# Optimization experiments

Measured on AMD Instinct MI355X. Metric: run time of the kernel, lower is better.

## Reference

```python
import jax, jax.numpy as jnp
import numpy as np

K = 499  # kernel_size


def setup_inputs() -> dict:
    key = jax.random.key(0)
    k1, k2 = jax.random.split(key)
    B, F, T = 32, 64, 8000
    # nonnegative spectrogram input, shape (B, 1, F, T)
    x = jax.random.uniform(k1, (B, 1, F, T), dtype=jnp.float32)
    a = 0.90 + 0.099 * jax.random.uniform(k2, (F,), dtype=jnp.float32)
    w = jnp.ones((F,), dtype=jnp.float32)
    return {"x": x, "a": a, "w": w}


def _build_kernel(a, w, dtype):
    # powers[f, k] = a_f ** k, k = 0..K-2
    F = a.shape[0]
    powers = a[:, None] ** jnp.arange(K - 1, dtype=dtype)  # (F, K-1)
    C = 1.0 / powers.sum(axis=1)                            # (F,)
    neg = (-C * w)[:, None] * powers                        # (F, K-1)
    # pre-flip kernel = [1, neg_0, ..., neg_{K-2}]; flipped -> [neg_{K-2}, ..., neg_0, 1]
    kern = jnp.concatenate([neg[:, ::-1], jnp.ones((F, 1), dtype)], axis=1)  # (F, K)
    return kern[:, None, :]  # (F, 1, K) OIH, groups = F


def reference(x, a, w):
    dtype = x.dtype
    kern = _build_kernel(a.astype(dtype), w.astype(dtype), dtype)
    xs = x[:, 0]  # (B, F, T)
    # replicate (edge) pad on the left by K-1 along time
    xp = jnp.pad(xs, ((0, 0), (0, 0), (K - 1, 0)), mode="edge")
    y = jax.lax.conv_general_dilated(
        xp, kern,
        window_strides=(1,), padding="VALID",
        dimension_numbers=("NCH", "OIH", "NCH"),
        feature_group_count=xs.shape[1],
    )  # (B, F, T)
    return jnp.abs(y)[:, None]  # (B, 1, F, T)
```

## Files before the change

### kernel.cpp

```cpp
#include <hip/hip_runtime.h>
#include <math.h>


constexpr int T     = 8000;
constexpr int F     = 64;
constexpr int B     = 32;
constexpr int KM1   = 498;
constexpr int CHUNK = 512;
constexpr int HALF  = 4096;
constexpr int LXN   = HALF + CHUNK;

#define DPP_F(x, ctrl, rm) \
  __builtin_bit_cast(float, __builtin_amdgcn_update_dpp(0, __builtin_bit_cast(int, (x)), (ctrl), (rm), 0xf, false))

__device__ __forceinline__ double dpow(double b, int e) {
    double r = 1.0, p = b;
    while (e) { if (e & 1) r *= p; p *= p; e >>= 1; }
    return r;
}

__device__ __forceinline__ float powi(float base, int e) {
    float r = 1.0f, p = base;
    #pragma unroll
    for (int b = 0; b < 9; ++b) { r = (e & (1 << b)) ? r * p : r; p *= p; }
    return r;
}

__device__ __forceinline__ int swz(int i) { return i ^ (((i >> 5) & 7) << 2); }

__global__ __launch_bounds__(512, 4) void willmore_scan_kernel(
    const float* __restrict__ x, const float* __restrict__ a,
    const float* __restrict__ w, float* __restrict__ out)
{
    __shared__ float lx[LXN];
    __shared__ float cb[8];

    const int tid  = threadIdx.x;
    const int cl   = tid >> 6;
    const int lane = tid & 63;
    const int row  = blockIdx.x >> 1;
    const int half = blockIdx.x & 1;
    const int f    = row & (F - 1);
    const int h0   = half * HALF;

    const float* xr   = x   + (size_t)row * T;
    float*       orow = out + (size_t)row * T;

    const int t0   = h0 + cl * CHUNK;
    const int tb_u = t0 + 8 * lane;
    const int tb   = min(tb_u, T - 8);
    const int lb   = tb - h0 + CHUNK;

    const float4 m0 = *(const float4*)(xr + tb);
    const float4 m1 = *(const float4*)(xr + tb + 4);
    float4 hv;
    if (half && tid < 128)
        hv = *(const float4*)(xr + h0 - CHUNK + 4 * tid);

    const float af    = a[f];
    const float alane = powi(af, 8 * lane);
    const float wA    = powi(af, 8 * ((lane & 15) + 1));
    const float wB    = powi(af, 8 * ((lane & 31) + 1));

    if (tid == 0) {
        const double ad     = (double)af;
        const double a498d  = dpow(ad, KM1);
        const double sumgeo = (1.0 - a498d) / (1.0 - ad);
        const double r_d    = dpow(ad, 8);
        cb[0] = (float)(-a498d);
        cb[1] = (float)(1.0 / sumgeo) * w[f];
        cb[2] = (float)r_d;
        cb[3] = (float)(r_d * r_d);
        cb[4] = (float)dpow(r_d, 4);
        cb[5] = (float)dpow(r_d, 8);
        cb[6] = (float)(1.0 / r_d);
        cb[7] = (float)sumgeo;
    }

    *(float4*)(&lx[swz(lb)])     = m0;
    *(float4*)(&lx[swz(lb + 4)]) = m1;
    if (half && tid < 128)
        *(float4*)(&lx[swz(4 * tid)]) = hv;
    __syncthreads();

    const float na498 = cb[0], g  = cb[1], r1    = cb[2], r2 = cb[3],
                r4    = cb[4], r8 = cb[5], inv_r = cb[6];

    float S;
    if (half == 0 && cl == 0) {
        S = lx[swz(CHUNK)] * cb[7];
    } else {
        const int wl = cl * CHUNK + 8 * lane;
        const float4 w0 = *(const float4*)(&lx[swz(wl)]);
        const float4 w1 = *(const float4*)(&lx[swz(wl + 4)]);
        float ws8[8] = {w0.x, w0.y, w0.z, w0.w, w1.x, w1.y, w1.z, w1.w};
        #pragma unroll
        for (int i = 0; i < 8; ++i) { if (8 * lane + i < 14) ws8[i] = 0.0f; }
        float h = ws8[0];
        #pragma unroll
        for (int i = 1; i < 8; ++i) h = fmaf(h, af, ws8[i]);
        float contrib = powi(af, 504 - 8 * lane) * h;
        #pragma unroll
        for (int s = 1; s < 64; s <<= 1) contrib += __shfl_xor(contrib, s, 64);
        S = contrib;
    }

    const int lg = tb - KM1;
    float lv[8];
    if (half == 0 && cl == 0) {
        #pragma unroll
        for (int i = 0; i < 8; ++i) lv[i] = lx[swz(max(lg + i, 0) + CHUNK)];
    } else {
        const int ll = lg - h0 + CHUNK;
        #pragma unroll
        for (int i = 0; i < 4; ++i) {
            const float2 p = *(const float2*)(&lx[swz(ll + 2 * i)]);
            lv[2 * i]     = p.x;
            lv[2 * i + 1] = p.y;
        }
    }

    const float xv[8] = {m0.x, m0.y, m0.z, m0.w, m1.x, m1.y, m1.z, m1.w};
    float u[8];
    #pragma unroll
    for (int i = 0; i < 8; ++i) u[i] = fmaf(na498, lv[i], xv[i]);

    float q = u[0];
    #pragma unroll
    for (int i = 1; i < 8; ++i) q = fmaf(q, af, u[i]);

    float G = q;
    G = fmaf(r1, DPP_F(G, 0x111, 0xf), G);
    G = fmaf(r2, DPP_F(G, 0x112, 0xf), G);
    G = fmaf(r4, DPP_F(G, 0x114, 0xf), G);
    G = fmaf(r8, DPP_F(G, 0x118, 0xf), G);
    G = fmaf(wA, DPP_F(G, 0x142, 0xa), G);
    G = fmaf(wB, DPP_F(G, 0x143, 0xc), G);

    const float E = (G - q) * inv_r;

    float s = fmaf(alane, S, E);
    float y[8];
    #pragma unroll
    for (int i = 0; i < 8; ++i) {
        y[i] = fabsf(fmaf(-g, s, xv[i]));
        s = fmaf(af, s, u[i]);
    }

    if (tb_u <= T - 8) {
        *(float4*)(orow + tb)     = make_float4(y[0], y[1], y[2], y[3]);
        *(float4*)(orow + tb + 4) = make_float4(y[4], y[5], y[6], y[7]);
    }
}

extern "C" void kernel_launch(void* const* d_in, const int* in_sizes, int n_in,
                              void* d_out, int out_size, void* d_ws, size_t ws_size,
                              hipStream_t stream) {
    const float* x = (const float*)d_in[0];
    const float* a = (const float*)d_in[1];
    const float* w = (const float*)d_in[2];
    float* out = (float*)d_out;

    hipLaunchKernelGGL(willmore_scan_kernel, dim3(B * F * 2), dim3(512), 0, stream,
                       x, a, w, out);
}
```

Baseline: 113.2 us.

## Split rows into quarter blocks with XCD-aware remap and nontemporal stores

Each row is now handled by four 256-thread blocks covering 2048 samples each, instead of two 512-thread blocks covering 4096. Block IDs are remapped so consecutive hardware blocks, which are spread across the XCDs, stay on related rows. Output stores become nontemporal. The intent is better occupancy and less LDS per block, and keeping the streaming output from polluting the cache. The cost is more redundant halo loads and more per-block setup work.

Measured after the change: 112.5 us. Within noise of the previous version (-0.6%).

```diff
diff --git a/kernel.cpp b/kernel.cpp
--- a/kernel.cpp
+++ b/kernel.cpp
@@ -7,8 +7,10 @@
 constexpr int B     = 32;
 constexpr int KM1   = 498;
 constexpr int CHUNK = 512;
-constexpr int HALF  = 4096;
-constexpr int LXN   = HALF + CHUNK;
+constexpr int QUART = 2048;
+constexpr int LXN   = QUART + CHUNK;
+
+typedef float vfloat4 __attribute__((ext_vector_type(4)));
 
 #define DPP_F(x, ctrl, rm) \
   __builtin_bit_cast(float, __builtin_amdgcn_update_dpp(0, __builtin_bit_cast(int, (x)), (ctrl), (rm), 0xf, false))
@@ -28,34 +30,37 @@
 
 __device__ __forceinline__ int swz(int i) { return i ^ (((i >> 5) & 7) << 2); }
 
-__global__ __launch_bounds__(512, 4) void willmore_scan_kernel(
+__global__ __launch_bounds__(256, 6) void willmore_scan_kernel(
     const float* __restrict__ x, const float* __restrict__ a,
     const float* __restrict__ w, float* __restrict__ out)
 {
     __shared__ float lx[LXN];
     __shared__ float cb[8];
 
+    const int bid  = blockIdx.x;
+    const int qid  = ((bid & 7) << 10) | (bid >> 3);
+
     const int tid  = threadIdx.x;
     const int cl   = tid >> 6;
     const int lane = tid & 63;
-    const int row  = blockIdx.x >> 1;
-    const int half = blockIdx.x & 1;
+    const int row  = qid >> 2;
+    const int qpos = qid & 3;
     const int f    = row & (F - 1);
-    const int h0   = half * HALF;
+    const int q0   = qpos * QUART;
 
     const float* xr   = x   + (size_t)row * T;
     float*       orow = out + (size_t)row * T;
 
-    const int t0   = h0 + cl * CHUNK;
+    const int t0   = q0 + cl * CHUNK;
     const int tb_u = t0 + 8 * lane;
     const int tb   = min(tb_u, T - 8);
-    const int lb   = tb - h0 + CHUNK;
+    const int lb   = tb - q0 + CHUNK;
 
     const float4 m0 = *(const float4*)(xr + tb);
     const float4 m1 = *(const float4*)(xr + tb + 4);
     float4 hv;
-    if (half && tid < 128)
-        hv = *(const float4*)(xr + h0 - CHUNK + 4 * tid);
+    if (qpos && tid < 128)
+        hv = *(const float4*)(xr + q0 - CHUNK + 4 * tid);
 
     const float af    = a[f];
     const float alane = powi(af, 8 * lane);
@@ -79,7 +84,7 @@
 
     *(float4*)(&lx[swz(lb)])     = m0;
     *(float4*)(&lx[swz(lb + 4)]) = m1;
-    if (half && tid < 128)
+    if (qpos && tid < 128)
         *(float4*)(&lx[swz(4 * tid)]) = hv;
     __syncthreads();
 
@@ -87,7 +92,7 @@
                 r4    = cb[4], r8 = cb[5], inv_r = cb[6];
 
     float S;
-    if (half == 0 && cl == 0) {
+    if (qpos == 0 && cl == 0) {
         S = lx[swz(CHUNK)] * cb[7];
     } else {
         const int wl = cl * CHUNK + 8 * lane;
@@ -107,11 +112,11 @@
 
     const int lg = tb - KM1;
     float lv[8];
-    if (half == 0 && cl == 0) {
+    if (qpos == 0 && cl == 0) {
         #pragma unroll
         for (int i = 0; i < 8; ++i) lv[i] = lx[swz(max(lg + i, 0) + CHUNK)];
     } else {
-        const int ll = lg - h0 + CHUNK;
+        const int ll = lg - q0 + CHUNK;
         #pragma unroll
         for (int i = 0; i < 4; ++i) {
             const float2 p = *(const float2*)(&lx[swz(ll + 2 * i)]);
@@ -148,8 +153,10 @@
     }
 
     if (tb_u <= T - 8) {
-        *(float4*)(orow + tb)     = make_float4(y[0], y[1], y[2], y[3]);
-        *(float4*)(orow + tb + 4) = make_float4(y[4], y[5], y[6], y[7]);
+        const vfloat4 o0 = {y[0], y[1], y[2], y[3]};
+        const vfloat4 o1 = {y[4], y[5], y[6], y[7]};
+        __builtin_nontemporal_store(o0, (vfloat4*)(orow + tb));
+        __builtin_nontemporal_store(o1, (vfloat4*)(orow + tb + 4));
     }
 }
 
@@ -161,6 +168,6 @@
     const float* w = (const float*)d_in[2];
     float* out = (float*)d_out;
 
-    hipLaunchKernelGGL(willmore_scan_kernel, dim3(B * F * 2), dim3(512), 0, stream,
+    hipLaunchKernelGGL(willmore_scan_kernel, dim3(B * F * 4), dim3(256), 0, stream,
                        x, a, w, out);
 }
```
